# Kernel optimization log

Measured on AMD Instinct MI355X. Metric: run time of the kernel, lower is better.

Reference implementation:

```python
import jax, jax.numpy as jnp
import numpy as np

E, R, D = 4096, 64, 256
LRELU_ALPHA = 0.2

def setup_inputs() -> dict:
    key = jax.random.key(0)
    k1, k2, k3, k4, k5 = jax.random.split(key, 5)
    h = jax.random.normal(k1, (E, D), dtype=jnp.float32)
    r = jax.random.normal(k2, (R, D), dtype=jnp.float32)
    adj_agg = jax.random.normal(k3, (E, R), dtype=jnp.float32)
    lim = 1.0 / np.sqrt(D)
    W_lin = jax.random.uniform(k4, (D, 1), jnp.float32, -lim, lim)  # torch Linear(in_features, 1)
    b_lin = jax.random.uniform(k5, (1,), jnp.float32, -lim, lim)
    return {"h": h, "r": r, "adj_agg": adj_agg, "W_lin": W_lin, "b_lin": b_lin}

def reference(h, r, adj_agg, W_lin, b_lin):
    # h: (E, D), r: (R, D), adj_agg: (E, R)
    adj = jax.nn.softmax(adj_agg, axis=1)
    # (h.repeat(1,R).view(R*E,-1) * r.repeat(E,1)).view(E,R,-1) == h[e]*r[j]
    a_input = h[:, None, :] * r[None, :, :]              # (E, R, D)
    att = adj[:, :, None] * a_input                      # (E, R, D)
    att = jnp.where(att >= 0, att, LRELU_ALPHA * att)    # LeakyReLU
    att_E = jax.nn.softmax(att, axis=0)                  # softmax over entities
    att_R = jax.nn.softmax(att, axis=1)                  # softmax over relations
    # dropout is identity in eval mode
    alpha = (att_R @ W_lin + b_lin).reshape(R, E, 1)     # faithful reshape (not transpose)
    alpha = jax.nn.softmax(alpha, axis=1)
    h_prime = jnp.sum(att_E * h[:, None, :], axis=1)     # (E, D)
    r_prime = jnp.sum(att_R * r[None, :, :], axis=0)     # (R, D)
    return jax.nn.elu(h_prime), jax.nn.elu(r_prime), alpha
```

## Files before the change

kernel.cpp:

```cpp
#include <hip/hip_runtime.h>


#define EN 4096
#define RN 64
#define DN 256
#define JT 16
#define NJT (RN/JT)
#define LOG2E 1.44269504088896340736f
#define CHA 8
#define CHB 8

__device__ __forceinline__ float ex2(float x){ return __builtin_amdgcn_exp2f(x); }

template<int CTRL>
__device__ __forceinline__ float dpp_add(float v){
  int m = __builtin_amdgcn_update_dpp(0, __float_as_int(v), CTRL, 0xf, 0xf, true);
  return v + __int_as_float(m);
}
__device__ __forceinline__ float row16_sum(float v){
  v = dpp_add<0x111>(v);
  v = dpp_add<0x112>(v);
  v = dpp_add<0x114>(v);
  v = dpp_add<0x118>(v);
  return v;
}

__global__ __launch_bounds__(256) void k_adj(const float* __restrict__ adj,
                                             float* __restrict__ s2){
  const int lane = threadIdx.x & 63;
  const int e = blockIdx.x*4 + (threadIdx.x >> 6);
  float a = adj[e*RN + lane];
  float ev = ex2(a * LOG2E);
  float s = ev;
  #pragma unroll
  for(int off = 32; off > 0; off >>= 1) s += __shfl_xor(s, off, 64);
  s2[e*RN + lane] = ev * (LOG2E / s);
}

__global__ __launch_bounds__(256,4) void kA(const float* __restrict__ h,
                                            const float* __restrict__ r,
                                            const float* __restrict__ s2,
                                            float* __restrict__ invlR,
                                            float* __restrict__ lE){
  const int d = threadIdx.x;
  const int e0 = blockIdx.x * CHA;
  __shared__ float s2s[CHA*RN];
  #pragma unroll
  for(int k = 0; k < CHA*RN/256; k++) s2s[k*256 + d] = s2[e0*RN + k*256 + d];
  __syncthreads();

  float lR[CHA];
  #pragma unroll
  for(int ee = 0; ee < CHA; ee++) lR[ee] = 0.f;

  #pragma unroll
  for(int jt = 0; jt < NJT; jt++){
    float rcol[JT], lEacc[JT];
    #pragma unroll
    for(int jj = 0; jj < JT; jj++){ rcol[jj] = r[(jt*JT+jj)*DN + d]; lEacc[jj] = 0.f; }
    #pragma unroll
    for(int ee = 0; ee < CHA; ee++){
      const float he = h[(e0+ee)*DN + d];
      #pragma unroll
      for(int jj = 0; jj < JT; jj++){
        float t  = s2s[ee*RN + jt*JT + jj] * he * rcol[jj];
        float ev = ex2(fmaxf(t, 0.2f*t));
        lR[ee]   += ev;
        lEacc[jj] += ev;
      }
    }
    #pragma unroll
    for(int jj = 0; jj < JT; jj++) atomicAdd(&lE[(jt*JT+jj)*DN + d], lEacc[jj]);
  }
  #pragma unroll
  for(int ee = 0; ee < CHA; ee++) invlR[(e0+ee)*DN + d] = 1.0f / lR[ee];
}

__global__ __launch_bounds__(256,4) void kB(const float* __restrict__ h,
                                            const float* __restrict__ r,
                                            const float* __restrict__ s2,
                                            const float* __restrict__ invlR,
                                            const float* __restrict__ lE,
                                            const float* __restrict__ W,
                                            float* __restrict__ hout,
                                            float* __restrict__ alog,
                                            float* __restrict__ racc_g){
  const int tid  = threadIdx.x;
  const int lane = tid & 63;
  const int grp  = tid >> 4;
  const int e0   = blockIdx.x * CHB;
  __shared__ float s2s[CHB*RN];
  __shared__ float apart[CHB*16*20];
  #pragma unroll
  for(int k = 0; k < CHB*RN/256; k++) s2s[k*256 + tid] = s2[e0*RN + k*256 + tid];
  __syncthreads();

  const float wd = W[tid];
  float sE[CHB];
  #pragma unroll
  for(int ee = 0; ee < CHB; ee++) sE[ee] = 0.f;

  #pragma unroll
  for(int jt = 0; jt < NJT; jt++){
    float rcol[JT], ile[JT], rAcc[JT];
    #pragma unroll
    for(int jj = 0; jj < JT; jj++){
      const int j = jt*JT + jj;
      rcol[jj] = r[j*DN + tid];
      ile[jj]  = 1.0f / lE[j*DN + tid];
      rAcc[jj] = 0.f;
    }
    for(int ee = 0; ee < CHB; ee++){
      const int e = e0 + ee;
      const float he = h[e*DN + tid];
      const float il = invlR[e*DN + tid];
      const float u  = il * wd;
      #pragma unroll
      for(int jg = 0; jg < JT/4; jg++){
        float4 st;
        #pragma unroll
        for(int jj4 = 0; jj4 < 4; jj4++){
          const int jj = jg*4 + jj4;
          float t  = s2s[ee*RN + jt*JT + jj] * he * rcol[jj];
          float ev = ex2(fmaxf(t, 0.2f*t));
          rAcc[jj] = fmaf(ev, il, rAcc[jj]);
          sE[ee]   = fmaf(ev, ile[jj], sE[ee]);
          float rs = row16_sum(ev * u);
          if(jj4==0) st.x = rs; else if(jj4==1) st.y = rs;
          else if(jj4==2) st.z = rs; else st.w = rs;
        }
        if((lane & 15) == 15){
          *reinterpret_cast<float4*>(&apart[(ee*16 + grp)*20 + jg*4]) = st;
        }
      }
    }
    __syncthreads();
    if(tid < CHB*JT){
      const int ee = tid >> 4, jj = tid & 15;
      float sum = 0.f;
      #pragma unroll
      for(int g = 0; g < 16; g++) sum += apart[(ee*16 + g)*20 + jj];
      alog[(e0+ee)*RN + jt*JT + jj] = sum;
    }
    __syncthreads();
    #pragma unroll
    for(int jj = 0; jj < JT; jj++) atomicAdd(&racc_g[(jt*JT+jj)*DN + tid], rAcc[jj]);
  }
  #pragma unroll
  for(int ee = 0; ee < CHB; ee++){
    const int e = e0 + ee;
    float hp = h[e*DN + tid] * sE[ee];
    hout[e*DN + tid] = hp > 0.f ? hp : (ex2(hp*LOG2E) - 1.0f);
  }
}

__global__ __launch_bounds__(256) void kR(const float* __restrict__ r,
                                          const float* __restrict__ racc,
                                          float* __restrict__ rout){
  int i = blockIdx.x*256 + threadIdx.x;
  float v = r[i] * racc[i];
  rout[i] = v > 0.f ? v : (ex2(v*LOG2E) - 1.0f);
}

__global__ __launch_bounds__(256) void kAlpha(const float* __restrict__ alog,
                                              float* __restrict__ aout){
  const int rr = blockIdx.x, tid = threadIdx.x;
  const float* __restrict__ row = alog + rr*EN;
  float exv[16]; float s = 0.f;
  #pragma unroll
  for(int k = 0; k < 16; k++){
    float v = ex2(row[k*256 + tid] * LOG2E);
    exv[k] = v; s += v;
  }
  #pragma unroll
  for(int off = 32; off > 0; off >>= 1) s += __shfl_xor(s, off, 64);
  __shared__ float wsum[4];
  if((tid & 63) == 0) wsum[tid>>6] = s;
  __syncthreads();
  float inv = 1.0f / (wsum[0] + wsum[1] + wsum[2] + wsum[3]);
  float* __restrict__ orow = aout + rr*EN;
  #pragma unroll
  for(int k = 0; k < 16; k++) orow[k*256 + tid] = exv[k] * inv;
}

extern "C" void kernel_launch(void* const* d_in, const int* in_sizes, int n_in,
                              void* d_out, int out_size, void* d_ws, size_t ws_size,
                              hipStream_t stream){
  (void)in_sizes; (void)n_in; (void)out_size; (void)ws_size;
  const float* h   = (const float*)d_in[0];
  const float* r   = (const float*)d_in[1];
  const float* adj = (const float*)d_in[2];
  const float* W   = (const float*)d_in[3];

  float* ws    = (float*)d_ws;
  float* s2    = ws;
  float* invlR = s2 + EN*RN;
  float* lE    = invlR + EN*DN;
  float* racc  = lE + RN*DN;
  float* alog  = racc + RN*DN;

  float* hout = (float*)d_out;
  float* rout = hout + EN*DN;
  float* aout = rout + RN*DN;

  hipMemsetAsync(lE, 0, size_t(RN*DN*2)*sizeof(float), stream);

  k_adj <<<EN/4,      256, 0, stream>>>(adj, s2);
  kA    <<<EN/CHA,    256, 0, stream>>>(h, r, s2, invlR, lE);
  kB    <<<EN/CHB,    256, 0, stream>>>(h, r, s2, invlR, lE, W, hout, alog, racc);
  kR    <<<RN*DN/256, 256, 0, stream>>>(r, racc, rout);
  kAlpha<<<RN,        256, 0, stream>>>(alog, aout);
}
```

Before: 180.0 us.

## Fuse adjacency softmax into main kernels and merge r-output into alpha kernel

Removes the separate adjacency-softmax kernel by recomputing the row softmax into shared memory inside both kA and kB, halving the entity chunk per block to 4 so one wave maps to one row. It also merges the r-prime ELU kernel into the alpha softmax kernel, uses hardware reciprocal instead of division, and reads the shared-memory scale factors as float4. This cuts two launches and the s2 workspace round trip. In exchange the softmax is computed twice, the grid doubles, and there are twice as many atomic adds into lE and racc, with slightly lower reciprocal precision.

```diff
diff --git a/kernel.cpp b/kernel.cpp
--- a/kernel.cpp
+++ b/kernel.cpp
@@ -7,10 +7,12 @@
 #define JT 16
 #define NJT (RN/JT)
 #define LOG2E 1.44269504088896340736f
-#define CHA 8
-#define CHB 8
+#define CH 4
+
+static_assert(CH == 4, "adj-softmax prologue maps one wave per e-row; needs CH==4");
 
 __device__ __forceinline__ float ex2(float x){ return __builtin_amdgcn_exp2f(x); }
+__device__ __forceinline__ float rcpf(float x){ return __builtin_amdgcn_rcpf(x); }
 
 template<int CTRL>
 __device__ __forceinline__ float dpp_add(float v){
@@ -25,33 +27,31 @@
   return v;
 }
 
-__global__ __launch_bounds__(256) void k_adj(const float* __restrict__ adj,
-                                             float* __restrict__ s2){
-  const int lane = threadIdx.x & 63;
-  const int e = blockIdx.x*4 + (threadIdx.x >> 6);
-  float a = adj[e*RN + lane];
+__device__ __forceinline__ void adj_sm(const float* __restrict__ adj, int e0,
+                                       float* __restrict__ s2s, int tid){
+  const int w = tid >> 6, lane = tid & 63;
+  float a  = adj[(e0 + w)*RN + lane];
   float ev = ex2(a * LOG2E);
-  float s = ev;
+  float s  = ev;
   #pragma unroll
   for(int off = 32; off > 0; off >>= 1) s += __shfl_xor(s, off, 64);
-  s2[e*RN + lane] = ev * (LOG2E / s);
+  s2s[w*RN + lane] = ev * (LOG2E * rcpf(s));
 }
 
 __global__ __launch_bounds__(256,4) void kA(const float* __restrict__ h,
                                             const float* __restrict__ r,
-                                            const float* __restrict__ s2,
+                                            const float* __restrict__ adj,
                                             float* __restrict__ invlR,
                                             float* __restrict__ lE){
-  const int d = threadIdx.x;
-  const int e0 = blockIdx.x * CHA;
-  __shared__ float s2s[CHA*RN];
-  #pragma unroll
-  for(int k = 0; k < CHA*RN/256; k++) s2s[k*256 + d] = s2[e0*RN + k*256 + d];
+  const int d  = threadIdx.x;
+  const int e0 = blockIdx.x * CH;
+  __shared__ float s2s[CH*RN];
+  adj_sm(adj, e0, s2s, d);
   __syncthreads();
 
-  float lR[CHA];
-  #pragma unroll
-  for(int ee = 0; ee < CHA; ee++) lR[ee] = 0.f;
+  float lR[CH];
+  #pragma unroll
+  for(int ee = 0; ee < CH; ee++) lR[ee] = 0.f;
 
   #pragma unroll
   for(int jt = 0; jt < NJT; jt++){
@@ -59,26 +59,32 @@
     #pragma unroll
     for(int jj = 0; jj < JT; jj++){ rcol[jj] = r[(jt*JT+jj)*DN + d]; lEacc[jj] = 0.f; }
     #pragma unroll
-    for(int ee = 0; ee < CHA; ee++){
+    for(int ee = 0; ee < CH; ee++){
       const float he = h[(e0+ee)*DN + d];
       #pragma unroll
-      for(int jj = 0; jj < JT; jj++){
-        float t  = s2s[ee*RN + jt*JT + jj] * he * rcol[jj];
-        float ev = ex2(fmaxf(t, 0.2f*t));
-        lR[ee]   += ev;
-        lEacc[jj] += ev;
+      for(int jg = 0; jg < JT/4; jg++){
+        const float4 s4 = *reinterpret_cast<const float4*>(&s2s[ee*RN + jt*JT + jg*4]);
+        #pragma unroll
+        for(int jj4 = 0; jj4 < 4; jj4++){
+          const int jj = jg*4 + jj4;
+          const float sv = (jj4==0)?s4.x:(jj4==1)?s4.y:(jj4==2)?s4.z:s4.w;
+          float t  = sv * he * rcol[jj];
+          float ev = ex2(fmaxf(t, 0.2f*t));
+          lR[ee]    += ev;
+          lEacc[jj] += ev;
+        }
       }
     }
     #pragma unroll
     for(int jj = 0; jj < JT; jj++) atomicAdd(&lE[(jt*JT+jj)*DN + d], lEacc[jj]);
   }
   #pragma unroll
-  for(int ee = 0; ee < CHA; ee++) invlR[(e0+ee)*DN + d] = 1.0f / lR[ee];
+  for(int ee = 0; ee < CH; ee++) invlR[(e0+ee)*DN + d] = rcpf(lR[ee]);
 }
 
 __global__ __launch_bounds__(256,4) void kB(const float* __restrict__ h,
                                             const float* __restrict__ r,
-                                            const float* __restrict__ s2,
+                                            const float* __restrict__ adj,
                                             const float* __restrict__ invlR,
                                             const float* __restrict__ lE,
                                             const float* __restrict__ W,
@@ -88,17 +94,16 @@
   const int tid  = threadIdx.x;
   const int lane = tid & 63;
   const int grp  = tid >> 4;
-  const int e0   = blockIdx.x * CHB;
-  __shared__ float s2s[CHB*RN];
-  __shared__ float apart[CHB*16*20];
-  #pragma unroll
-  for(int k = 0; k < CHB*RN/256; k++) s2s[k*256 + tid] = s2[e0*RN + k*256 + tid];
+  const int e0   = blockIdx.x * CH;
+  __shared__ float s2s[CH*RN];
+  __shared__ float apart[CH*16*20];
+  adj_sm(adj, e0, s2s, tid);
   __syncthreads();
 
   const float wd = W[tid];
-  float sE[CHB];
-  #pragma unroll
-  for(int ee = 0; ee < CHB; ee++) sE[ee] = 0.f;
+  float sE[CH];
+  #pragma unroll
+  for(int ee = 0; ee < CH; ee++) sE[ee] = 0.f;
 
   #pragma unroll
   for(int jt = 0; jt < NJT; jt++){
@@ -107,21 +112,23 @@
     for(int jj = 0; jj < JT; jj++){
       const int j = jt*JT + jj;
       rcol[jj] = r[j*DN + tid];
-      ile[jj]  = 1.0f / lE[j*DN + tid];
+      ile[jj]  = rcpf(lE[j*DN + tid]);
       rAcc[jj] = 0.f;
     }
-    for(int ee = 0; ee < CHB; ee++){
+    for(int ee = 0; ee < CH; ee++){
       const int e = e0 + ee;
       const float he = h[e*DN + tid];
       const float il = invlR[e*DN + tid];
       const float u  = il * wd;
       #pragma unroll
       for(int jg = 0; jg < JT/4; jg++){
+        const float4 s4 = *reinterpret_cast<const float4*>(&s2s[ee*RN + jt*JT + jg*4]);
         float4 st;
         #pragma unroll
         for(int jj4 = 0; jj4 < 4; jj4++){
           const int jj = jg*4 + jj4;
-          float t  = s2s[ee*RN + jt*JT + jj] * he * rcol[jj];
+          const float sv = (jj4==0)?s4.x:(jj4==1)?s4.y:(jj4==2)?s4.z:s4.w;
+          float t  = sv * he * rcol[jj];
           float ev = ex2(fmaxf(t, 0.2f*t));
           rAcc[jj] = fmaf(ev, il, rAcc[jj]);
           sE[ee]   = fmaf(ev, ile[jj], sE[ee]);
@@ -135,7 +142,7 @@
       }
     }
     __syncthreads();
-    if(tid < CHB*JT){
+    if(tid < CH*JT){
       const int ee = tid >> 4, jj = tid & 15;
       float sum = 0.f;
       #pragma unroll
@@ -147,24 +154,24 @@
     for(int jj = 0; jj < JT; jj++) atomicAdd(&racc_g[(jt*JT+jj)*DN + tid], rAcc[jj]);
   }
   #pragma unroll
-  for(int ee = 0; ee < CHB; ee++){
+  for(int ee = 0; ee < CH; ee++){
     const int e = e0 + ee;
     float hp = h[e*DN + tid] * sE[ee];
     hout[e*DN + tid] = hp > 0.f ? hp : (ex2(hp*LOG2E) - 1.0f);
   }
 }
 
-__global__ __launch_bounds__(256) void kR(const float* __restrict__ r,
-                                          const float* __restrict__ racc,
-                                          float* __restrict__ rout){
-  int i = blockIdx.x*256 + threadIdx.x;
-  float v = r[i] * racc[i];
-  rout[i] = v > 0.f ? v : (ex2(v*LOG2E) - 1.0f);
-}
-
-__global__ __launch_bounds__(256) void kAlpha(const float* __restrict__ alog,
-                                              float* __restrict__ aout){
+__global__ __launch_bounds__(256) void kAlphaR(const float* __restrict__ alog,
+                                               const float* __restrict__ r,
+                                               const float* __restrict__ racc,
+                                               float* __restrict__ aout,
+                                               float* __restrict__ rout){
   const int rr = blockIdx.x, tid = threadIdx.x;
+  {
+    const int i = rr*DN + tid;
+    float v = r[i] * racc[i];
+    rout[i] = v > 0.f ? v : (ex2(v*LOG2E) - 1.0f);
+  }
   const float* __restrict__ row = alog + rr*EN;
   float exv[16]; float s = 0.f;
   #pragma unroll
@@ -193,8 +200,7 @@
   const float* W   = (const float*)d_in[3];
 
   float* ws    = (float*)d_ws;
-  float* s2    = ws;
-  float* invlR = s2 + EN*RN;
+  float* invlR = ws;
   float* lE    = invlR + EN*DN;
   float* racc  = lE + RN*DN;
   float* alog  = racc + RN*DN;
@@ -205,9 +211,7 @@
 
   hipMemsetAsync(lE, 0, size_t(RN*DN*2)*sizeof(float), stream);
 
-  k_adj <<<EN/4,      256, 0, stream>>>(adj, s2);
-  kA    <<<EN/CHA,    256, 0, stream>>>(h, r, s2, invlR, lE);
-  kB    <<<EN/CHB,    256, 0, stream>>>(h, r, s2, invlR, lE, W, hout, alog, racc);
-  kR    <<<RN*DN/256, 256, 0, stream>>>(r, racc, rout);
-  kAlpha<<<RN,        256, 0, stream>>>(alog, aout);
-}
+  kA     <<<EN/CH, 256, 0, stream>>>(h, r, adj, invlR, lE);
+  kB     <<<EN/CH, 256, 0, stream>>>(h, r, adj, invlR, lE, W, hout, alog, racc);
+  kAlphaR<<<RN,    256, 0, stream>>>(alog, r, racc, aout, rout);
+}
```

Result: slower. 418.9 us (+132.8%).
